# Kernel optimization log

Hardware: AMD Instinct MI355X
Metric: run time of the kernel (lower is better)

## Reference

```python
import jax, jax.numpy as jnp
import numpy as np

K = 3  # kernel size


def _bilinear_sample(x, px, py):
    """Bilinear sample x:[b,c,h,w] at pixel coords px,py:[b,t,h,w].
    Zeros padding, align_corners=True semantics (coords are raw pixel coords).
    Returns [b,c,t,h,w]."""
    b, c, h, w = x.shape
    x0 = jnp.floor(px)
    y0 = jnp.floor(py)
    wx1 = px - x0
    wx0 = 1.0 - wx1
    wy1 = py - y0
    wy0 = 1.0 - wy1
    xf = x.reshape(b, c, h * w)

    def gather(xi, yi):
        valid = (xi >= 0) & (xi <= w - 1) & (yi >= 0) & (yi <= h - 1)
        xi_c = jnp.clip(xi, 0, w - 1).astype(jnp.int32)
        yi_c = jnp.clip(yi, 0, h - 1).astype(jnp.int32)
        idx = (yi_c * w + xi_c).reshape(b, 1, -1)  # [b,1,t*h*w]
        v = jnp.take_along_axis(xf, idx, axis=2).reshape(b, c, *xi.shape[1:])
        return v * valid[:, None].astype(x.dtype)

    out = (gather(x0, y0) * (wx0 * wy0)[:, None]
           + gather(x0 + 1, y0) * (wx1 * wy0)[:, None]
           + gather(x0, y0 + 1) * (wx0 * wy1)[:, None]
           + gather(x0 + 1, y0 + 1) * (wx1 * wy1)[:, None])
    return out


def setup_inputs() -> dict:
    key = jax.random.key(0)
    k1, k2, k3 = jax.random.split(key, 3)
    b, c, h, w = 4, 64, 128, 128
    out_c = 64
    x = jax.random.normal(k1, (b, c, h, w), dtype=jnp.float32)
    offset = jax.random.normal(k2, (b, 2 * K * K, h, w), dtype=jnp.float32)
    weight = jax.random.normal(k3, (out_c, c, K, K), dtype=jnp.float32) * 0.05
    bias = jnp.zeros((out_c,), dtype=jnp.float32)
    return {"x": x, "offset": offset, "weight": weight, "bias": bias}


def reference(x, offset, weight, bias):
    b, c, h, w = x.shape
    kk = K * K
    # base integer grid (x along width, y along height)
    yy, xx = jnp.meshgrid(jnp.arange(h, dtype=x.dtype), jnp.arange(w, dtype=x.dtype), indexing='ij')
    off = offset.reshape(b, kk, 2, h, w)
    # grid_sample with align_corners=True inverts the module's normalization,
    # so effective sampling coords are simply base + offset in pixel space.
    px = xx[None, None] + off[:, :, 0]  # [b,kk,h,w]
    py = yy[None, None] + off[:, :, 1]
    sampled = _bilinear_sample(x, px, py)  # [b,c,kk,h,w]
    w2 = weight.reshape(weight.shape[0], c, kk)  # [o,c,kk]
    out = jnp.einsum('oct,bcthw->bohw', w2, sampled)
    return out + bias[None, :, None, None]
```

## Files before the change

kernel.cpp:

```cpp
#include <hip/hip_runtime.h>
#include <cstddef>

#define BH 4
#define CH 64
#define OH 64
#define HH 128
#define WW 128
#define KK 9
#define HW (HH * WW)

typedef __attribute__((ext_vector_type(8))) short short8;
typedef __attribute__((ext_vector_type(4))) float f32x4;
typedef __attribute__((ext_vector_type(2))) float f32x2;
typedef __attribute__((ext_vector_type(4))) unsigned int uint4v;
typedef __attribute__((ext_vector_type(4))) unsigned short ushort4v;

__device__ __forceinline__ unsigned short f2bf(float f) {
    unsigned u = __float_as_uint(f);
    u += 0x7fffu + ((u >> 16) & 1u);
    return (unsigned short)(u >> 16);
}
__device__ __forceinline__ f32x2 bf2x2(unsigned d) {
    f32x2 r;
    r.x = __uint_as_float(d << 16);
    r.y = __uint_as_float(d & 0xffff0000u);
    return r;
}
__device__ __forceinline__ unsigned pack_bf2(f32x2 v) {
    unsigned u0 = __float_as_uint(v.x);
    u0 += 0x7fffu + ((u0 >> 16) & 1u);
    unsigned u1 = __float_as_uint(v.y);
    u1 += 0x7fffu + ((u1 >> 16) & 1u);
    return __builtin_amdgcn_perm(u1, u0, 0x07060302);
}
__device__ __forceinline__ uint4v combine4(uint4v c00, uint4v c10, uint4v c01, uint4v c11,
                                           float w00, float w10, float w01, float w11) {
    f32x2 W00 = {w00, w00}, W10 = {w10, w10}, W01 = {w01, w01}, W11 = {w11, w11};
    uint4v r;
#pragma unroll
    for (int j = 0; j < 4; ++j) {
        f32x2 s = W00 * bf2x2(c00[j]) + W10 * bf2x2(c10[j])
                + W01 * bf2x2(c01[j]) + W11 * bf2x2(c11[j]);
        r[j] = pack_bf2(s);
    }
    return r;
}

__global__ __launch_bounds__(256) void dcl_prep(const float* __restrict__ x,
                                                const float* __restrict__ wgt,
                                                unsigned short* __restrict__ xt,
                                                unsigned short* __restrict__ wtb) {
    if (blockIdx.x < 1024) {
        __shared__ float tile[64][65];
        int chunk = blockIdx.x;
        int b = chunk >> 8;
        int hw0 = (chunk & 255) * 64;
        int tid = threadIdx.x;
        int tx = tid & 63;
        int ty = tid >> 6;
        const float* xb = x + (size_t)b * CH * HW;
#pragma unroll
        for (int c = ty; c < 64; c += 4)
            tile[c][tx] = xb[(size_t)c * HW + hw0 + tx];
        __syncthreads();
        unsigned short* xtb = xt + ((size_t)b << 20);
        int c4 = (tid & 15) * 4;
        int p0 = tid >> 4;
#pragma unroll
        for (int it = 0; it < 4; ++it) {
            int pxl = p0 + it * 16;
            ushort4v v = { f2bf(tile[c4 + 0][pxl]), f2bf(tile[c4 + 1][pxl]),
                           f2bf(tile[c4 + 2][pxl]), f2bf(tile[c4 + 3][pxl]) };
            *(ushort4v*)(xtb + (size_t)(hw0 + pxl) * CH + c4) = v;
        }
    } else {
        int idx = (blockIdx.x - 1024) * 256 + threadIdx.x;
        int j  = idx & 7;
        int l  = (idx >> 3) & 63;
        int nt = (idx >> 9) & 3;
        int ks = idx >> 11;
        int k = ks * 32 + ((l >> 4) * 8) + j;
        int n = nt * 16 + (l & 15);
        int c = k & 63;
        int t = k >> 6;
        wtb[idx] = f2bf(wgt[(n * CH + c) * KK + t]);
    }
}

#define NW 8
#define B_WORDS 18432
#define OSLICE_WORDS 1040

__global__ __launch_bounds__(512, 4) void dcl_main(
        const unsigned short* __restrict__ xt,
        const float* __restrict__ offset,
        const unsigned short* __restrict__ wtb,
        const float* __restrict__ bias,
        float* __restrict__ out) {
    __shared__ int smem[B_WORDS];
    int tid = threadIdx.x;
    int lane = tid & 63;
    int wave = tid >> 6;

    int b  = blockIdx.x >> 7;
    int t7 = blockIdx.x & 127;
    int x0 = (t7 & 7) << 4;
    int y0 = (t7 >> 3) << 3;
    int m = lane & 15;
    int quad = lane >> 4;
    int qoff = quad * 16;
    int y = y0 + wave;
    int pm = x0 + m;

    const char* xtb = (const char*)xt;
    const float* ob = offset + (((size_t)(b * 18)) << 14) + (y << 7) + pm;
    float pxf = (float)pm;
    float pyf = (float)y;

    float oxv[9], oyv[9];
#pragma unroll
    for (int t = 0; t < 9; ++t) {
        oxv[t] = ob[(size_t)(2 * t) << 14];
        oyv[t] = ob[(size_t)(2 * t + 1) << 14];
    }

    {
        const uint4v* bsrc = (const uint4v*)wtb;
        uint4v* bdst = (uint4v*)smem;
#pragma unroll
        for (int r = 0; r < 9; ++r)
            bdst[r * 512 + tid] = bsrc[r * 512 + tid];
    }

    f32x4 acc[4];
#pragma unroll
    for (int i = 0; i < 4; ++i) acc[i] = (f32x4)(0.f);

    const short8* bl = (const short8*)smem;

    __syncthreads();

#pragma unroll
    for (int t = 0; t < 9; ++t) {
        float fx = pxf + oxv[t];
        float fy = pyf + oyv[t];
        float x0f = floorf(fx), y0f = floorf(fy);
        float wx1 = fx - x0f, wy1 = fy - y0f;
        float wx0 = 1.0f - wx1, wy0 = 1.0f - wy1;
        int ix0 = (int)x0f, iy0 = (int)y0f;
        int ix1 = ix0 + 1, iy1 = iy0 + 1;
        bool vx0 = (unsigned)ix0 < (unsigned)WW;
        bool vx1 = (unsigned)ix1 < (unsigned)WW;
        bool vy0 = (unsigned)iy0 < (unsigned)HH;
        bool vy1 = (unsigned)iy1 < (unsigned)HH;
        float w00 = (vx0 && vy0) ? wx0 * wy0 : 0.0f;
        float w10 = (vx1 && vy0) ? wx1 * wy0 : 0.0f;
        float w01 = (vx0 && vy1) ? wx0 * wy1 : 0.0f;
        float w11 = (vx1 && vy1) ? wx1 * wy1 : 0.0f;
        int cx0 = min(max(ix0, 0), WW - 1), cx1 = min(max(ix1, 0), WW - 1);
        int cy0 = min(max(iy0, 0), HH - 1), cy1 = min(max(iy1, 0), HH - 1);
        int base = b << 14;
        int o00 = ((base + (cy0 << 7) + cx0) << 7) + qoff;
        int o10 = ((base + (cy0 << 7) + cx1) << 7) + qoff;
        int o01 = ((base + (cy1 << 7) + cx0) << 7) + qoff;
        int o11 = ((base + (cy1 << 7) + cx1) << 7) + qoff;

        uint4v c00a = *(const uint4v*)(xtb + o00);
        uint4v c10a = *(const uint4v*)(xtb + o10);
        uint4v c01a = *(const uint4v*)(xtb + o01);
        uint4v c11a = *(const uint4v*)(xtb + o11);
        uint4v c00b = *(const uint4v*)(xtb + o00 + 64);
        uint4v c10b = *(const uint4v*)(xtb + o10 + 64);
        uint4v c01b = *(const uint4v*)(xtb + o01 + 64);
        uint4v c11b = *(const uint4v*)(xtb + o11 + 64);
        uint4v ra = combine4(c00a, c10a, c01a, c11a, w00, w10, w01, w11);
        uint4v rb = combine4(c00b, c10b, c01b, c11b, w00, w10, w01, w11);
        short8 aa = __builtin_bit_cast(short8, ra);
        short8 ab = __builtin_bit_cast(short8, rb);

        int ks = 2 * t;
#pragma unroll
        for (int nt = 0; nt < 4; ++nt)
            acc[nt] = __builtin_amdgcn_mfma_f32_16x16x32_bf16(
                aa, bl[(ks * 4 + nt) * 64 + lane], acc[nt], 0, 0, 0);
#pragma unroll
        for (int nt = 0; nt < 4; ++nt)
            acc[nt] = __builtin_amdgcn_mfma_f32_16x16x32_bf16(
                ab, bl[((ks + 1) * 4 + nt) * 64 + lane], acc[nt], 0, 0, 0);
    }

    __syncthreads();
    float* o_w = (float*)smem + wave * OSLICE_WORDS;
#pragma unroll
    for (int nt = 0; nt < 4; ++nt)
#pragma unroll
        for (int reg = 0; reg < 4; ++reg)
            o_w[(quad * 4 + reg) * 65 + nt * 16 + m] = acc[nt][reg];
    __syncthreads();

    const float* os = (const float*)smem;
#pragma unroll
    for (int j = tid; j < 64 * 128; j += 512) {
        int o = j >> 7;
        int p = j & 127;
        int row = p >> 4, xx = p & 15;
        float v = os[row * OSLICE_WORDS + xx * 65 + o] + bias[o];
        out[(((size_t)(b * OH + o)) << 14) + ((y0 + row) << 7) + x0 + xx] = v;
    }
}

extern "C" void kernel_launch(void* const* d_in, const int* in_sizes, int n_in,
                              void* d_out, int out_size, void* d_ws, size_t ws_size,
                              hipStream_t stream) {
    const float* x      = (const float*)d_in[0];
    const float* offset = (const float*)d_in[1];
    const float* weight = (const float*)d_in[2];
    const float* bias   = (const float*)d_in[3];
    float* out = (float*)d_out;

    unsigned short* xt  = (unsigned short*)d_ws;
    unsigned short* wtb = (unsigned short*)((char*)d_ws + (size_t)BH * HW * CH * 2);

    dcl_prep<<<1024 + 144, 256, 0, stream>>>(x, weight, xt, wtb);
    dcl_main<<<BH * HH, 512, 0, stream>>>(xt, offset, wtb, bias, out);
}
```

Measured before the change: 112.2 us.

## Shrink blocks to 256 threads and double-buffer weight slices in LDS per tap

The main kernel now runs 256-thread blocks that cover 4 rows by 16 pixels each, which doubles the grid. It no longer stages the full 72 KB weight matrix in shared memory. Instead it keeps a 16 KB double buffer and prefetches each tap's weight slice into registers while the current tap is sampled and multiplied. The goal is to cut LDS use so more blocks fit per CU and the weight load overlaps compute. The cost is a barrier every tap iteration and the loss of full unrolling.

```diff
diff --git a/kernel.cpp b/kernel.cpp
--- a/kernel.cpp
+++ b/kernel.cpp
@@ -87,25 +87,23 @@
     }
 }
 
-#define NW 8
-#define B_WORDS 18432
-#define OSLICE_WORDS 1040
-
-__global__ __launch_bounds__(512, 4) void dcl_main(
+#define SMEM_INTS 4352
+
+__global__ __launch_bounds__(256, 4) void dcl_main(
         const unsigned short* __restrict__ xt,
         const float* __restrict__ offset,
         const unsigned short* __restrict__ wtb,
         const float* __restrict__ bias,
         float* __restrict__ out) {
-    __shared__ int smem[B_WORDS];
+    __shared__ __align__(16) int smem[SMEM_INTS];
     int tid = threadIdx.x;
     int lane = tid & 63;
     int wave = tid >> 6;
 
-    int b  = blockIdx.x >> 7;
-    int t7 = blockIdx.x & 127;
-    int x0 = (t7 & 7) << 4;
-    int y0 = (t7 >> 3) << 3;
+    int b  = blockIdx.x >> 8;
+    int t8 = blockIdx.x & 255;
+    int x0 = (t8 & 7) << 4;
+    int y0 = (t8 >> 3) << 2;
     int m = lane & 15;
     int quad = lane >> 4;
     int qoff = quad * 16;
@@ -124,24 +122,28 @@
         oyv[t] = ob[(size_t)(2 * t + 1) << 14];
     }
 
+    const uint4v* bsrc = (const uint4v*)wtb;
+
     {
-        const uint4v* bsrc = (const uint4v*)wtb;
-        uint4v* bdst = (uint4v*)smem;
-#pragma unroll
-        for (int r = 0; r < 9; ++r)
-            bdst[r * 512 + tid] = bsrc[r * 512 + tid];
+        uint4v* dst = (uint4v*)smem;
+        dst[tid]       = bsrc[tid];
+        dst[tid + 256] = bsrc[tid + 256];
     }
 
     f32x4 acc[4];
 #pragma unroll
     for (int i = 0; i < 4; ++i) acc[i] = (f32x4)(0.f);
 
-    const short8* bl = (const short8*)smem;
-
     __syncthreads();
 
-#pragma unroll
+#pragma unroll 1
     for (int t = 0; t < 9; ++t) {
+        uint4v r0, r1;
+        if (t < 8) {
+            r0 = bsrc[(t + 1) * 512 + tid];
+            r1 = bsrc[(t + 1) * 512 + 256 + tid];
+        }
+
         float fx = pxf + oxv[t];
         float fy = pyf + oyv[t];
         float x0f = floorf(fx), y0f = floorf(fy);
@@ -178,19 +180,25 @@
         short8 aa = __builtin_bit_cast(short8, ra);
         short8 ab = __builtin_bit_cast(short8, rb);
 
-        int ks = 2 * t;
+        const short8* bl = (const short8*)(smem + (t & 1) * 2048);
 #pragma unroll
         for (int nt = 0; nt < 4; ++nt)
             acc[nt] = __builtin_amdgcn_mfma_f32_16x16x32_bf16(
-                aa, bl[(ks * 4 + nt) * 64 + lane], acc[nt], 0, 0, 0);
+                aa, bl[nt * 64 + lane], acc[nt], 0, 0, 0);
 #pragma unroll
         for (int nt = 0; nt < 4; ++nt)
             acc[nt] = __builtin_amdgcn_mfma_f32_16x16x32_bf16(
-                ab, bl[((ks + 1) * 4 + nt) * 64 + lane], acc[nt], 0, 0, 0);
-    }
-
-    __syncthreads();
-    float* o_w = (float*)smem + wave * OSLICE_WORDS;
+                ab, bl[(4 + nt) * 64 + lane], acc[nt], 0, 0, 0);
+
+        if (t < 8) {
+            uint4v* dst = (uint4v*)(smem + ((t + 1) & 1) * 2048);
+            dst[tid]       = r0;
+            dst[tid + 256] = r1;
+        }
+        __syncthreads();
+    }
+
+    float* o_w = (float*)smem + wave * 1040;
 #pragma unroll
     for (int nt = 0; nt < 4; ++nt)
 #pragma unroll
@@ -200,11 +208,11 @@
 
     const float* os = (const float*)smem;
 #pragma unroll
-    for (int j = tid; j < 64 * 128; j += 512) {
-        int o = j >> 7;
-        int p = j & 127;
+    for (int j = tid; j < 64 * 64; j += 256) {
+        int o = j >> 6;
+        int p = j & 63;
         int row = p >> 4, xx = p & 15;
-        float v = os[row * OSLICE_WORDS + xx * 65 + o] + bias[o];
+        float v = os[row * 1040 + xx * 65 + o] + bias[o];
         out[(((size_t)(b * OH + o)) << 14) + ((y0 + row) << 7) + x0 + xx] = v;
     }
 }
@@ -222,5 +230,5 @@
     unsigned short* wtb = (unsigned short*)((char*)d_ws + (size_t)BH * HW * CH * 2);
 
     dcl_prep<<<1024 + 144, 256, 0, stream>>>(x, weight, xt, wtb);
-    dcl_main<<<BH * HH, 512, 0, stream>>>(xt, offset, wtb, bias, out);
-}
+    dcl_main<<<(BH * HW) / 64, 256, 0, stream>>>(xt, offset, wtb, bias, out);
+}
```

Measured after the change: 115.8 us. 3.1% more time.
